# Kernel tuning notes

Measured on AMD Instinct MI355X. Metric: run time of the kernel, lower is better.

Reference implementation:

```python
import jax, jax.numpy as jnp
import numpy as np

N, H = 131072, 256          # rows, hidden_dim
P, K_OCC, K_SUBJ = 16, 8, 16  # phases, occurrences per phase, subjects per occurrence
O = P * K_OCC               # 128 total occurrence classes
S = O * K_SUBJ              # 2048 total subject classes


def setup_inputs() -> dict:
    key = jax.random.key(0)
    ks = jax.random.split(key, 10)
    X = jax.random.normal(ks[0], (N, H), jnp.float32)
    X_phase = jax.random.randint(ks[1], (N,), 0, P)
    X_occ_local = jax.random.randint(ks[2], (N,), 0, K_OCC)
    X_subj_local = jax.random.randint(ks[3], (N,), 0, K_SUBJ)
    sc = 1.0 / np.sqrt(H)  # nn.Linear default init range
    W_phase = jax.random.uniform(ks[4], (P, H), jnp.float32, -sc, sc)
    b_phase = jax.random.uniform(ks[5], (P,), jnp.float32, -sc, sc)
    W_p2o = jax.random.uniform(ks[6], (O, H), jnp.float32, -sc, sc)      # stacked phase_to_occurrence Linears
    b_p2o = jax.random.uniform(ks[7], (O,), jnp.float32, -sc, sc)
    W_o2s = jax.random.uniform(ks[8], (S, H), jnp.float32, -sc, sc)      # stacked occurrence_to_subj Linears
    b_o2s = jax.random.uniform(ks[9], (S,), jnp.float32, -sc, sc)
    return {
        "X": X, "W_phase": W_phase, "b_phase": b_phase,
        "W_p2o": W_p2o, "b_p2o": b_p2o, "W_o2s": W_o2s, "b_o2s": b_o2s,
        "X_phase": X_phase, "X_occ_local": X_occ_local, "X_subj_local": X_subj_local,
    }


def reference(X, W_phase, b_phase, W_p2o, b_p2o, W_o2s, b_o2s,
              X_phase, X_occ_local, X_subj_local):
    n = X.shape[0]
    rows = jnp.arange(n)

    # phase head: softmax over all P phases, pick the true phase prob
    phase_proba = jax.nn.softmax(X @ W_phase.T + b_phase, axis=1)[rows, X_phase]  # [N]

    # occurrence head: per-sample small Linear chosen by phase key -> compute all
    # stacked logits once, gather the phase's K_OCC-block, softmax within block
    occ_logits = (X @ W_p2o.T + b_p2o).reshape(n, P, K_OCC)[rows, X_phase]        # [N, K_OCC]
    occ_proba = jax.nn.softmax(occ_logits, axis=1)[rows, X_occ_local]             # [N]

    # subject head: same pattern keyed by global occurrence id
    X_occurrence = X_phase * K_OCC + X_occ_local                                   # global occ ids
    subj_logits = (X @ W_o2s.T + b_o2s).reshape(n, O, K_SUBJ)[rows, X_occurrence]  # [N, K_SUBJ]
    subj_proba = jax.nn.softmax(subj_logits, axis=1)[rows, X_subj_local]           # [N]

    po = phase_proba * occ_proba
    return (phase_proba, po, po * subj_proba)
```

## Files before the change

kernel.cpp:

```cpp
#include <hip/hip_runtime.h>

#define H_ 256
#define P_ 16
#define KOCC 8
#define KSUBJ 16
#define O_ 128
#define CAPMAX 2048

typedef __attribute__((ext_vector_type(8))) __bf16 bf16x8;
typedef __attribute__((ext_vector_type(4))) float f32x4;

__device__ __forceinline__ bf16x8 load_bf8(const float* p) {
  float4 a = *(const float4*)p;
  float4 b = *(const float4*)(p + 4);
  bf16x8 r;
  r[0] = (__bf16)a.x; r[1] = (__bf16)a.y; r[2] = (__bf16)a.z; r[3] = (__bf16)a.w;
  r[4] = (__bf16)b.x; r[5] = (__bf16)b.y; r[6] = (__bf16)b.z; r[7] = (__bf16)b.w;
  return r;
}

__device__ __forceinline__ bf16x8 cvt_bf8(float4 a, float4 b) {
  bf16x8 r;
  r[0] = (__bf16)a.x; r[1] = (__bf16)a.y; r[2] = (__bf16)a.z; r[3] = (__bf16)a.w;
  r[4] = (__bf16)b.x; r[5] = (__bf16)b.y; r[6] = (__bf16)b.z; r[7] = (__bf16)b.w;
  return r;
}

__global__ __launch_bounds__(1024) void scatter_kernel(
    const int* __restrict__ xp, const int* __restrict__ xo,
    int* counts, int* brows, int n, int cap) {
  __shared__ int hist[O_];
  __shared__ int basev[O_];
  int tid = threadIdx.x;
  if (tid < O_) hist[tid] = 0;
  __syncthreads();
  int base_i = blockIdx.x * 4096 + tid;
  int be[4], pos[4];
#pragma unroll
  for (int e = 0; e < 4; ++e) {
    int i = base_i + e * 1024;
    pos[e] = -1;
    if (i < n) {
      be[e] = xp[i] * KOCC + xo[i];
      pos[e] = atomicAdd(&hist[be[e]], 1);
    }
  }
  __syncthreads();
  if (tid < O_) basev[tid] = atomicAdd(&counts[tid], hist[tid]);
  __syncthreads();
#pragma unroll
  for (int e = 0; e < 4; ++e) {
    if (pos[e] >= 0) {
      int idx = basev[be[e]] + pos[e];
      if (idx < cap) brows[be[e] * cap + idx] = base_i + e * 1024;
    }
  }
}

__global__ __launch_bounds__(256, 4) void hsm_main(
    const float* __restrict__ X,
    const float* __restrict__ Wp, const float* __restrict__ bp,
    const float* __restrict__ Wo, const float* __restrict__ bo,
    const float* __restrict__ Ws, const float* __restrict__ bs,
    const int* __restrict__ subj,
    const int* __restrict__ counts, const int* __restrict__ brows,
    float* __restrict__ out, int n, int cap) {
  int b = blockIdx.x & 127;
  int chunk = blockIdx.x >> 7;
  int count = counts[b];
  if (count > cap) count = cap;
  int p = b >> 3;
  int occl = b & 7;

  __shared__ __bf16 Bf[3 * 8 * 64 * 8];
  __shared__ float S[4][3 * 16 * 16];

  {
    int t = threadIdx.x;
#pragma unroll
    for (int it = 0; it < 6; ++it) {
      int fid = it * 256 + t;
      int lane_f = fid & 63;
      int hk = fid >> 6;
      int head = hk >> 3, kk = hk & 7;
      int colf = lane_f & 15, quadf = lane_f >> 4;
      const float* src;
      if (head == 0)      src = Wp + colf * H_;
      else if (head == 1) src = Wo + (p * KOCC + (colf & 7)) * H_;
      else                src = Ws + (b * KSUBJ + colf) * H_;
      bf16x8 v = load_bf8(src + kk * 32 + quadf * 8);
      *(bf16x8*)&Bf[(size_t)fid * 8] = v;
    }
  }
  __syncthreads();

  int lane = threadIdx.x & 63;
  int wave = threadIdx.x >> 6;
  int col = lane & 15;
  int quad = lane >> 4;

  const int* brow_b = brows + b * cap;
  const bf16x8* Bfrag = (const bf16x8*)Bf;
  float* Sw = S[wave];

  int rr = lane & 15;
  int hh = lane >> 4;

  bool v1 = col < KOCC;
  float bias0 = bp[col];
  float bias1 = v1 ? bo[p * KOCC + col] : 0.0f;
  float bias2 = bs[b * KSUBJ + col];

  for (int base = chunk * 64 + wave * 16; base < count; base += 1024) {
    int rem = count - base;
    int rida = brow_b[base + (col < rem ? col : rem - 1)];
    int subjv = subj[rida];
    const float* xr = X + (size_t)rida * H_ + quad * 8;

    float4 ta[8], tb[8];
#pragma unroll
    for (int kk = 0; kk < 8; ++kk) {
      const float4* s = (const float4*)(xr + kk * 32);
      ta[kk] = s[0];
      tb[kk] = s[1];
    }
    __builtin_amdgcn_sched_barrier(0);

    f32x4 acc0 = {0.f, 0.f, 0.f, 0.f};
    f32x4 acc1 = {0.f, 0.f, 0.f, 0.f};
    f32x4 acc2 = {0.f, 0.f, 0.f, 0.f};
#pragma unroll
    for (int kk = 0; kk < 8; ++kk) {
      bf16x8 a = cvt_bf8(ta[kk], tb[kk]);
      acc0 = __builtin_amdgcn_mfma_f32_16x16x32_bf16(a, Bfrag[kk * 64 + lane], acc0, 0, 0, 0);
      acc1 = __builtin_amdgcn_mfma_f32_16x16x32_bf16(a, Bfrag[(8 + kk) * 64 + lane], acc1, 0, 0, 0);
      acc2 = __builtin_amdgcn_mfma_f32_16x16x32_bf16(a, Bfrag[(16 + kk) * 64 + lane], acc2, 0, 0, 0);
    }

#pragma unroll
    for (int r = 0; r < 4; ++r) {
      int row = quad * 4 + r;
      Sw[0 * 256 + row * 16 + col] = acc0[r] + bias0;
      Sw[1 * 256 + row * 16 + col] = acc1[r] + bias1;
      Sw[2 * 256 + row * 16 + col] = acc2[r] + bias2;
    }

    int tsub_r = __shfl(subjv, rr);

    float prob;
    {
      const float* Lx = Sw + (hh < 3 ? hh * 256 : 0) + rr * 16;
      float4 c0 = *(const float4*)(Lx + 0);
      float4 c1 = *(const float4*)(Lx + 4);
      float4 c2 = *(const float4*)(Lx + 8);
      float4 c3 = *(const float4*)(Lx + 12);
      int tgt = (hh == 0) ? p : ((hh == 1) ? occl : tsub_r);
      float lt = Lx[tgt];
      float den;
      if (hh == 1) {
        den = __expf(c0.x) + __expf(c0.y) + __expf(c0.z) + __expf(c0.w)
            + __expf(c1.x) + __expf(c1.y) + __expf(c1.z) + __expf(c1.w);
      } else {
        den = __expf(c0.x) + __expf(c0.y) + __expf(c0.z) + __expf(c0.w)
            + __expf(c1.x) + __expf(c1.y) + __expf(c1.z) + __expf(c1.w)
            + __expf(c2.x) + __expf(c2.y) + __expf(c2.z) + __expf(c2.w)
            + __expf(c3.x) + __expf(c3.y) + __expf(c3.z) + __expf(c3.w);
      }
      prob = __expf(lt) / den;
    }
    float p1v = __shfl(prob, (lane + 16) & 63);
    float p2v = __shfl(prob, (lane + 32) & 63);
    if (hh == 0 && rr < rem) {
      float po = prob * p1v;
      out[rida] = prob;
      out[n + rida] = po;
      out[2 * n + rida] = po * p2v;
    }
  }
}

extern "C" void kernel_launch(void* const* d_in, const int* in_sizes, int n_in,
                              void* d_out, int out_size, void* d_ws, size_t ws_size,
                              hipStream_t stream) {
  const float* X  = (const float*)d_in[0];
  const float* Wp = (const float*)d_in[1];
  const float* bp = (const float*)d_in[2];
  const float* Wo = (const float*)d_in[3];
  const float* bo = (const float*)d_in[4];
  const float* Ws = (const float*)d_in[5];
  const float* bs = (const float*)d_in[6];
  const int* xp   = (const int*)d_in[7];
  const int* xo   = (const int*)d_in[8];
  const int* xs   = (const int*)d_in[9];
  float* out = (float*)d_out;
  int n = in_sizes[7];

  int* wsI = (int*)d_ws;
  int* counts = wsI;
  int* brows = wsI + 128;
  long avail = (long)(ws_size / 4) - 128;
  int cap = (int)(avail / O_);
  if (cap > CAPMAX) cap = CAPMAX;
  if (cap < 1) cap = 1;

  hipMemsetAsync(counts, 0, O_ * sizeof(int), stream);
  scatter_kernel<<<dim3((n + 4095) / 4096), dim3(1024), 0, stream>>>(xp, xo, counts, brows, n, cap);
  hsm_main<<<dim3(O_ * 16), dim3(256), 0, stream>>>(X, Wp, bp, Wo, bo, Ws, bs, xs,
                                                    counts, brows, out, n, cap);
}
```

Before: 222.6 us.

## Pre-permute X into bucket-contiguous bf16 buffer before main MFMA kernel

Adds a permute kernel that reads X in row order, converts it to bf16 and writes each row to its bucket slot in a workspace buffer. The main kernel then reads contiguous bf16 rows instead of gathering scattered fp32 rows, which halves its read bytes and removes the in-loop conversion. The cost is an extra full pass over X, an extra write of a bf16 copy, one more kernel launch, and a fixed CAP layout that no longer checks the workspace size.

```diff
diff --git a/kernel.cpp b/kernel.cpp
--- a/kernel.cpp
+++ b/kernel.cpp
@@ -5,9 +5,10 @@
 #define KOCC 8
 #define KSUBJ 16
 #define O_ 128
-#define CAPMAX 2048
+#define CAP 2048
 
 typedef __attribute__((ext_vector_type(8))) __bf16 bf16x8;
+typedef __attribute__((ext_vector_type(4))) __bf16 bf16x4;
 typedef __attribute__((ext_vector_type(4))) float f32x4;
 
 __device__ __forceinline__ bf16x8 load_bf8(const float* p) {
@@ -19,16 +20,9 @@
   return r;
 }
 
-__device__ __forceinline__ bf16x8 cvt_bf8(float4 a, float4 b) {
-  bf16x8 r;
-  r[0] = (__bf16)a.x; r[1] = (__bf16)a.y; r[2] = (__bf16)a.z; r[3] = (__bf16)a.w;
-  r[4] = (__bf16)b.x; r[5] = (__bf16)b.y; r[6] = (__bf16)b.z; r[7] = (__bf16)b.w;
-  return r;
-}
-
 __global__ __launch_bounds__(1024) void scatter_kernel(
     const int* __restrict__ xp, const int* __restrict__ xo,
-    int* counts, int* brows, int n, int cap) {
+    int* counts, int* brows, int* dfull, int n) {
   __shared__ int hist[O_];
   __shared__ int basev[O_];
   int tid = threadIdx.x;
@@ -51,24 +45,57 @@
 #pragma unroll
   for (int e = 0; e < 4; ++e) {
     if (pos[e] >= 0) {
+      int i = base_i + e * 1024;
       int idx = basev[be[e]] + pos[e];
-      if (idx < cap) brows[be[e] * cap + idx] = base_i + e * 1024;
+      if (idx < CAP) {
+        brows[be[e] * CAP + idx] = i;
+        dfull[i] = be[e] * CAP + idx;
+      } else {
+        dfull[i] = -1;
+      }
+    }
+  }
+}
+
+__global__ __launch_bounds__(256) void permute_kernel(
+    const float* __restrict__ X, const int* __restrict__ dfull,
+    __bf16* __restrict__ Xg, int n) {
+  int t = threadIdx.x;
+  int rl = t >> 6;
+  int slot = t & 63;
+  int rbase = blockIdx.x * 16;
+  int dst[4];
+  float4 v[4];
+#pragma unroll
+  for (int it = 0; it < 4; ++it) {
+    int r = rbase + it * 4 + rl;
+    dst[it] = dfull[r];
+    v[it] = *(const float4*)(X + (size_t)r * H_ + slot * 4);
+  }
+  __builtin_amdgcn_sched_barrier(0);
+#pragma unroll
+  for (int it = 0; it < 4; ++it) {
+    if (dst[it] >= 0) {
+      bf16x4 o;
+      o[0] = (__bf16)v[it].x; o[1] = (__bf16)v[it].y;
+      o[2] = (__bf16)v[it].z; o[3] = (__bf16)v[it].w;
+      *(bf16x4*)(Xg + (size_t)dst[it] * H_ + slot * 4) = o;
     }
   }
 }
 
 __global__ __launch_bounds__(256, 4) void hsm_main(
-    const float* __restrict__ X,
+    const __bf16* __restrict__ Xg,
     const float* __restrict__ Wp, const float* __restrict__ bp,
     const float* __restrict__ Wo, const float* __restrict__ bo,
     const float* __restrict__ Ws, const float* __restrict__ bs,
     const int* __restrict__ subj,
     const int* __restrict__ counts, const int* __restrict__ brows,
-    float* __restrict__ out, int n, int cap) {
+    float* __restrict__ out, int n) {
   int b = blockIdx.x & 127;
   int chunk = blockIdx.x >> 7;
   int count = counts[b];
-  if (count > cap) count = cap;
+  if (count > CAP) count = CAP;
   int p = b >> 3;
   int occl = b & 7;
 
@@ -99,7 +126,7 @@
   int col = lane & 15;
   int quad = lane >> 4;
 
-  const int* brow_b = brows + b * cap;
+  const int* brow_b = brows + b * CAP;
   const bf16x8* Bfrag = (const bf16x8*)Bf;
   float* Sw = S[wave];
 
@@ -113,17 +140,15 @@
 
   for (int base = chunk * 64 + wave * 16; base < count; base += 1024) {
     int rem = count - base;
-    int rida = brow_b[base + (col < rem ? col : rem - 1)];
+    int rowsel = base + (col < rem ? col : rem - 1);
+    int rida = brow_b[rowsel];
     int subjv = subj[rida];
-    const float* xr = X + (size_t)rida * H_ + quad * 8;
-
-    float4 ta[8], tb[8];
-#pragma unroll
-    for (int kk = 0; kk < 8; ++kk) {
-      const float4* s = (const float4*)(xr + kk * 32);
-      ta[kk] = s[0];
-      tb[kk] = s[1];
-    }
+    const __bf16* xr = Xg + ((size_t)b * CAP + rowsel) * H_;
+
+    bf16x8 af[8];
+#pragma unroll
+    for (int kk = 0; kk < 8; ++kk)
+      af[kk] = *(const bf16x8*)(xr + kk * 32 + quad * 8);
     __builtin_amdgcn_sched_barrier(0);
 
     f32x4 acc0 = {0.f, 0.f, 0.f, 0.f};
@@ -131,10 +156,9 @@
     f32x4 acc2 = {0.f, 0.f, 0.f, 0.f};
 #pragma unroll
     for (int kk = 0; kk < 8; ++kk) {
-      bf16x8 a = cvt_bf8(ta[kk], tb[kk]);
-      acc0 = __builtin_amdgcn_mfma_f32_16x16x32_bf16(a, Bfrag[kk * 64 + lane], acc0, 0, 0, 0);
-      acc1 = __builtin_amdgcn_mfma_f32_16x16x32_bf16(a, Bfrag[(8 + kk) * 64 + lane], acc1, 0, 0, 0);
-      acc2 = __builtin_amdgcn_mfma_f32_16x16x32_bf16(a, Bfrag[(16 + kk) * 64 + lane], acc2, 0, 0, 0);
+      acc0 = __builtin_amdgcn_mfma_f32_16x16x32_bf16(af[kk], Bfrag[kk * 64 + lane], acc0, 0, 0, 0);
+      acc1 = __builtin_amdgcn_mfma_f32_16x16x32_bf16(af[kk], Bfrag[(8 + kk) * 64 + lane], acc1, 0, 0, 0);
+      acc2 = __builtin_amdgcn_mfma_f32_16x16x32_bf16(af[kk], Bfrag[(16 + kk) * 64 + lane], acc2, 0, 0, 0);
     }
 
 #pragma unroll
@@ -198,13 +222,12 @@
   int* wsI = (int*)d_ws;
   int* counts = wsI;
   int* brows = wsI + 128;
-  long avail = (long)(ws_size / 4) - 128;
-  int cap = (int)(avail / O_);
-  if (cap > CAPMAX) cap = CAPMAX;
-  if (cap < 1) cap = 1;
+  int* dfull = wsI + 128 + O_ * CAP;
+  __bf16* Xg = (__bf16*)(wsI + 128 + O_ * CAP + n);
 
   hipMemsetAsync(counts, 0, O_ * sizeof(int), stream);
-  scatter_kernel<<<dim3((n + 4095) / 4096), dim3(1024), 0, stream>>>(xp, xo, counts, brows, n, cap);
-  hsm_main<<<dim3(O_ * 16), dim3(256), 0, stream>>>(X, Wp, bp, Wo, bo, Ws, bs, xs,
-                                                    counts, brows, out, n, cap);
-}
+  scatter_kernel<<<dim3((n + 4095) / 4096), dim3(1024), 0, stream>>>(xp, xo, counts, brows, dfull, n);
+  permute_kernel<<<dim3(n / 16), dim3(256), 0, stream>>>(X, dfull, Xg, n);
+  hsm_main<<<dim3(O_ * 16), dim3(256), 0, stream>>>(Xg, Wp, bp, Wo, bo, Ws, bs, xs,
+                                                    counts, brows, out, n);
+}
```

Result: slower. 249.8 us (+12.2%).

## Precompute bf16 weight fragments globally and use single-wave blocks with register-held B

Applied to the files above, without the earlier changes.

A new prep kernel converts the three heads' weight slices into bf16 MFMA fragments once per bucket and writes them to workspace. The main kernel becomes 64-thread blocks that load all 24 fragments into registers instead of every 256-thread block redoing the fp32 loads, conversion and shared-memory staging. The scatter kernel now also stores subject labels alongside row ids, so the main kernel avoids a dependent gather. X loads are split into two halves to reduce register pressure. The trade-off is an extra kernel launch, a fixed workspace capacity of 2048 rows per bucket that is no longer derived from the workspace size, and many more small blocks.

```diff
diff --git a/kernel.cpp b/kernel.cpp
--- a/kernel.cpp
+++ b/kernel.cpp
@@ -5,7 +5,7 @@
 #define KOCC 8
 #define KSUBJ 16
 #define O_ 128
-#define CAPMAX 2048
+#define CAP 2048
 
 typedef __attribute__((ext_vector_type(8))) __bf16 bf16x8;
 typedef __attribute__((ext_vector_type(4))) float f32x4;
@@ -28,7 +28,8 @@
 
 __global__ __launch_bounds__(1024) void scatter_kernel(
     const int* __restrict__ xp, const int* __restrict__ xo,
-    int* counts, int* brows, int n, int cap) {
+    const int* __restrict__ xs,
+    int* counts, int* brows, int* bsubj, int n) {
   __shared__ int hist[O_];
   __shared__ int basev[O_];
   int tid = threadIdx.x;
@@ -51,105 +52,117 @@
 #pragma unroll
   for (int e = 0; e < 4; ++e) {
     if (pos[e] >= 0) {
+      int i = base_i + e * 1024;
       int idx = basev[be[e]] + pos[e];
-      if (idx < cap) brows[be[e] * cap + idx] = base_i + e * 1024;
-    }
-  }
-}
-
-__global__ __launch_bounds__(256, 4) void hsm_main(
+      if (idx < CAP) {
+        brows[be[e] * CAP + idx] = i;
+        bsubj[be[e] * CAP + idx] = xs[i];
+      }
+    }
+  }
+}
+
+__global__ __launch_bounds__(256) void prep_frags(
+    const float* __restrict__ Wp, const float* __restrict__ Wo,
+    const float* __restrict__ Ws, bf16x8* __restrict__ Bg) {
+  int b = blockIdx.x;
+  int p = b >> 3;
+  int t = threadIdx.x;
+#pragma unroll
+  for (int it = 0; it < 6; ++it) {
+    int fid = it * 256 + t;
+    int lane_f = fid & 63;
+    int f = fid >> 6;
+    int head = f >> 3, kk = f & 7;
+    int colf = lane_f & 15, quadf = lane_f >> 4;
+    const float* src;
+    if (head == 0)      src = Wp + colf * H_;
+    else if (head == 1) src = Wo + (p * KOCC + (colf & 7)) * H_;
+    else                src = Ws + (b * KSUBJ + colf) * H_;
+    Bg[(b * 24 + f) * 64 + lane_f] = load_bf8(src + kk * 32 + quadf * 8);
+  }
+}
+
+__global__ __launch_bounds__(64, 2) void hsm_main(
     const float* __restrict__ X,
-    const float* __restrict__ Wp, const float* __restrict__ bp,
-    const float* __restrict__ Wo, const float* __restrict__ bo,
-    const float* __restrict__ Ws, const float* __restrict__ bs,
-    const int* __restrict__ subj,
+    const float* __restrict__ bp, const float* __restrict__ bo,
+    const float* __restrict__ bs,
     const int* __restrict__ counts, const int* __restrict__ brows,
-    float* __restrict__ out, int n, int cap) {
+    const int* __restrict__ bsubj, const bf16x8* __restrict__ Bg,
+    float* __restrict__ out, int n) {
   int b = blockIdx.x & 127;
   int chunk = blockIdx.x >> 7;
   int count = counts[b];
-  if (count > cap) count = cap;
+  if (count > CAP) count = CAP;
+  int base0 = chunk * 16;
+  if (base0 >= count) return;
   int p = b >> 3;
   int occl = b & 7;
 
-  __shared__ __bf16 Bf[3 * 8 * 64 * 8];
-  __shared__ float S[4][3 * 16 * 16];
-
-  {
-    int t = threadIdx.x;
-#pragma unroll
-    for (int it = 0; it < 6; ++it) {
-      int fid = it * 256 + t;
-      int lane_f = fid & 63;
-      int hk = fid >> 6;
-      int head = hk >> 3, kk = hk & 7;
-      int colf = lane_f & 15, quadf = lane_f >> 4;
-      const float* src;
-      if (head == 0)      src = Wp + colf * H_;
-      else if (head == 1) src = Wo + (p * KOCC + (colf & 7)) * H_;
-      else                src = Ws + (b * KSUBJ + colf) * H_;
-      bf16x8 v = load_bf8(src + kk * 32 + quadf * 8);
-      *(bf16x8*)&Bf[(size_t)fid * 8] = v;
-    }
-  }
-  __syncthreads();
-
-  int lane = threadIdx.x & 63;
-  int wave = threadIdx.x >> 6;
+  int lane = threadIdx.x;
   int col = lane & 15;
   int quad = lane >> 4;
 
-  const int* brow_b = brows + b * cap;
-  const bf16x8* Bfrag = (const bf16x8*)Bf;
-  float* Sw = S[wave];
-
-  int rr = lane & 15;
-  int hh = lane >> 4;
+  __shared__ float S[3 * 16 * 16];
+
+  bf16x8 Bf[24];
+#pragma unroll
+  for (int f = 0; f < 24; ++f) Bf[f] = Bg[(b * 24 + f) * 64 + lane];
 
   bool v1 = col < KOCC;
   float bias0 = bp[col];
   float bias1 = v1 ? bo[p * KOCC + col] : 0.0f;
   float bias2 = bs[b * KSUBJ + col];
-
-  for (int base = chunk * 64 + wave * 16; base < count; base += 1024) {
+  const int* brow_b = brows + b * CAP;
+  const int* bsub_b = bsubj + b * CAP;
+  int rr = lane & 15;
+  int hh = lane >> 4;
+
+  for (int base = base0; base < count; base += 1024) {
     int rem = count - base;
-    int rida = brow_b[base + (col < rem ? col : rem - 1)];
-    int subjv = subj[rida];
+    int rowsel = base + (col < rem ? col : rem - 1);
+    int rida = brow_b[rowsel];
+    int subjv = bsub_b[rowsel];
     const float* xr = X + (size_t)rida * H_ + quad * 8;
 
-    float4 ta[8], tb[8];
-#pragma unroll
-    for (int kk = 0; kk < 8; ++kk) {
-      const float4* s = (const float4*)(xr + kk * 32);
-      ta[kk] = s[0];
-      tb[kk] = s[1];
-    }
-    __builtin_amdgcn_sched_barrier(0);
+    bf16x8 af[8];
+#pragma unroll
+    for (int half = 0; half < 2; ++half) {
+      float4 ta[4], tb[4];
+#pragma unroll
+      for (int kk = 0; kk < 4; ++kk) {
+        const float4* s = (const float4*)(xr + (half * 4 + kk) * 32);
+        ta[kk] = s[0];
+        tb[kk] = s[1];
+      }
+      __builtin_amdgcn_sched_barrier(0);
+#pragma unroll
+      for (int kk = 0; kk < 4; ++kk) af[half * 4 + kk] = cvt_bf8(ta[kk], tb[kk]);
+    }
 
     f32x4 acc0 = {0.f, 0.f, 0.f, 0.f};
     f32x4 acc1 = {0.f, 0.f, 0.f, 0.f};
     f32x4 acc2 = {0.f, 0.f, 0.f, 0.f};
 #pragma unroll
     for (int kk = 0; kk < 8; ++kk) {
-      bf16x8 a = cvt_bf8(ta[kk], tb[kk]);
-      acc0 = __builtin_amdgcn_mfma_f32_16x16x32_bf16(a, Bfrag[kk * 64 + lane], acc0, 0, 0, 0);
-      acc1 = __builtin_amdgcn_mfma_f32_16x16x32_bf16(a, Bfrag[(8 + kk) * 64 + lane], acc1, 0, 0, 0);
-      acc2 = __builtin_amdgcn_mfma_f32_16x16x32_bf16(a, Bfrag[(16 + kk) * 64 + lane], acc2, 0, 0, 0);
+      acc0 = __builtin_amdgcn_mfma_f32_16x16x32_bf16(af[kk], Bf[kk], acc0, 0, 0, 0);
+      acc1 = __builtin_amdgcn_mfma_f32_16x16x32_bf16(af[kk], Bf[8 + kk], acc1, 0, 0, 0);
+      acc2 = __builtin_amdgcn_mfma_f32_16x16x32_bf16(af[kk], Bf[16 + kk], acc2, 0, 0, 0);
     }
 
 #pragma unroll
     for (int r = 0; r < 4; ++r) {
       int row = quad * 4 + r;
-      Sw[0 * 256 + row * 16 + col] = acc0[r] + bias0;
-      Sw[1 * 256 + row * 16 + col] = acc1[r] + bias1;
-      Sw[2 * 256 + row * 16 + col] = acc2[r] + bias2;
+      S[0 * 256 + row * 16 + col] = acc0[r] + bias0;
+      S[1 * 256 + row * 16 + col] = acc1[r] + bias1;
+      S[2 * 256 + row * 16 + col] = acc2[r] + bias2;
     }
 
     int tsub_r = __shfl(subjv, rr);
 
     float prob;
     {
-      const float* Lx = Sw + (hh < 3 ? hh * 256 : 0) + rr * 16;
+      const float* Lx = S + (hh < 3 ? hh * 256 : 0) + rr * 16;
       float4 c0 = *(const float4*)(Lx + 0);
       float4 c1 = *(const float4*)(Lx + 4);
       float4 c2 = *(const float4*)(Lx + 8);
@@ -198,13 +211,11 @@
   int* wsI = (int*)d_ws;
   int* counts = wsI;
   int* brows = wsI + 128;
-  long avail = (long)(ws_size / 4) - 128;
-  int cap = (int)(avail / O_);
-  if (cap > CAPMAX) cap = CAPMAX;
-  if (cap < 1) cap = 1;
+  int* bsubj = wsI + 128 + O_ * CAP;
+  bf16x8* Bg = (bf16x8*)(wsI + 128 + 2 * O_ * CAP);
 
   hipMemsetAsync(counts, 0, O_ * sizeof(int), stream);
-  scatter_kernel<<<dim3((n + 4095) / 4096), dim3(1024), 0, stream>>>(xp, xo, counts, brows, n, cap);
-  hsm_main<<<dim3(O_ * 16), dim3(256), 0, stream>>>(X, Wp, bp, Wo, bo, Ws, bs, xs,
-                                                    counts, brows, out, n, cap);
-}
+  scatter_kernel<<<dim3((n + 4095) / 4096), dim3(1024), 0, stream>>>(xp, xo, xs, counts, brows, bsubj, n);
+  prep_frags<<<dim3(O_), dim3(256), 0, stream>>>(Wp, Wo, Ws, Bg);
+  hsm_main<<<dim3(O_ * 64), dim3(64), 0, stream>>>(X, bp, bo, bs, counts, brows, bsubj, Bg, out, n);
+}
```

Result: slower. 231.0 us (+3.8%).
